# Kernel tuning notes

Measured on AMD Instinct MI355X. Metric: run time of the kernel, lower is better.

The kernel has to match this reference:

```python
import jax, jax.numpy as jnp
import numpy as np

B, S, D, H = 4, 1024, 768, 12
DH = D // H  # 64
ALPHA = 0.5
EPS = 1e-12


def setup_inputs() -> dict:
    key = jax.random.key(0)
    ks = jax.random.split(key, 12)
    s = 0.02
    return {
        "hidden_states": jax.random.normal(ks[0], (B, S, D), jnp.float32),
        "attention_mask": jnp.zeros((B, 1, 1, S), jnp.float32),
        "previous_attention": jax.random.uniform(ks[1], (B, H, S, S), jnp.float32),
        "Wq": jax.random.normal(ks[2], (D, D), jnp.float32) * s,
        "bq": jnp.zeros((D,), jnp.float32),
        "Wk": jax.random.normal(ks[3], (D, D), jnp.float32) * s,
        "bk": jnp.zeros((D,), jnp.float32),
        "Wv": jax.random.normal(ks[4], (D, D), jnp.float32) * s,
        "bv": jnp.zeros((D,), jnp.float32),
        "conv_w": jax.random.normal(ks[5], (H, H), jnp.float32) * 0.1,  # 1x1 conv over head channels
        "conv_b": jnp.zeros((H,), jnp.float32),
        "Wo": jax.random.normal(ks[6], (D, D), jnp.float32) * s,
        "bo": jnp.zeros((D,), jnp.float32),
        "ln_w": jnp.ones((D,), jnp.float32),
        "ln_b": jnp.zeros((D,), jnp.float32),
    }


def _split_heads(x):
    # [B,S,D] -> [B,H,S,DH]
    return x.reshape(B, S, H, DH).transpose(0, 2, 1, 3)


def reference(hidden_states, attention_mask, previous_attention,
              Wq, bq, Wk, bk, Wv, bv, conv_w, conv_b, Wo, bo, ln_w, ln_b):
    q = _split_heads(hidden_states @ Wq + bq)
    k = _split_heads(hidden_states @ Wk + bk)
    v = _split_heads(hidden_states @ Wv + bv)

    scores = jnp.einsum('bhqd,bhkd->bhqk', q, k) / jnp.sqrt(jnp.float32(DH))
    scores = scores + attention_mask
    probs = jax.nn.softmax(scores, axis=-1)

    # 1x1 conv over head channels on previous attention, mix, re-softmax
    prev = jnp.einsum('oi,biqk->boqk', conv_w, previous_attention) + conv_b[None, :, None, None]
    probs = jax.nn.softmax(ALPHA * prev + (1.0 - ALPHA) * probs, axis=-1)

    ctx = jnp.einsum('bhqk,bhkd->bhqd', probs, v)
    ctx = ctx.transpose(0, 2, 1, 3).reshape(B, S, D)

    out = ctx @ Wo + bo
    out = out + hidden_states
    u = out.mean(-1, keepdims=True)
    var = ((out - u) ** 2).mean(-1, keepdims=True)
    out = (out - u) / jnp.sqrt(var + EPS)
    return ln_w * out + ln_b
```

## Files before the change

### kernel.cpp

```cpp
#include <hip/hip_runtime.h>
#include <math.h>

#define BB 4
#define SS 1024
#define DD 768
#define HH 12
#define DHH 64

typedef __attribute__((ext_vector_type(8))) short bf16x8;
typedef __attribute__((ext_vector_type(4))) float f32x4;

__device__ __forceinline__ unsigned int f2bf(float f) {
    unsigned int u = __float_as_uint(f);
    return (u + 0x7FFFu + ((u >> 16) & 1u)) >> 16;
}
__device__ __forceinline__ float bf2f(unsigned int h) {
    return __uint_as_float(h << 16);
}

__device__ __forceinline__ void glds16(const void* g, void* l) {
    __builtin_amdgcn_global_load_lds(
        (const __attribute__((address_space(1))) void*)g,
        (__attribute__((address_space(3))) void*)l, 16, 0, 0);
}

__global__ __launch_bounds__(256)
void cvt_hidden_kernel(const float* __restrict__ src, unsigned short* __restrict__ dst)
{
    const int idx = (blockIdx.x * 256 + threadIdx.x) * 8;
    float4 a = *(const float4*)&src[idx];
    float4 b = *(const float4*)&src[idx + 4];
    uint4 p;
    p.x = f2bf(a.x) | (f2bf(a.y) << 16);
    p.y = f2bf(a.z) | (f2bf(a.w) << 16);
    p.z = f2bf(b.x) | (f2bf(b.y) << 16);
    p.w = f2bf(b.z) | (f2bf(b.w) << 16);
    *(uint4*)&dst[idx] = p;
}

__global__ __launch_bounds__(256)
void transpose_w_kernel(const float* __restrict__ Wq, const float* __restrict__ Wk,
                        const float* __restrict__ Wv, const float* __restrict__ Wo,
                        unsigned short* __restrict__ Wt)
{
    __shared__ float tile[32][33];
    const int t = threadIdx.x;
    const int kt = blockIdx.x, nt = blockIdx.y, w = blockIdx.z;
    const float* src = (w == 0) ? Wq : (w == 1) ? Wk : (w == 2) ? Wv : Wo;
    const int r = t >> 3, c4 = (t & 7) * 4;
    float4 v = *(const float4*)&src[(kt * 32 + r) * DD + nt * 32 + c4];
    tile[r][c4 + 0] = v.x; tile[r][c4 + 1] = v.y;
    tile[r][c4 + 2] = v.z; tile[r][c4 + 3] = v.w;
    __syncthreads();
    uint2 p;
    p.x = f2bf(tile[c4 + 0][r]) | (f2bf(tile[c4 + 1][r]) << 16);
    p.y = f2bf(tile[c4 + 2][r]) | (f2bf(tile[c4 + 3][r]) << 16);
    *(uint2*)&Wt[((size_t)w * DD + nt * 32 + r) * DD + kt * 32 + c4] = p;
}

__device__ __forceinline__ void gemm_core64(
    const char* __restrict__ Ag, const char* __restrict__ Bg,
    char* As, char* Bs, int tid, f32x4 (&acc)[2][2])
{
    const int lane = tid & 63;
    const int wr = (tid >> 7) & 1;
    const int wc = (tid >> 6) & 1;
    const int ldst = (tid & 192) << 4;

    for (int c = 0; c < 12; ++c) {
        const int kbyte = c * 128;
        #pragma unroll
        for (int i = 0; i < 2; ++i) {
            const int s = i * 256 + tid;
            const int row = s >> 3, kb = s & 7;
            const size_t off = (size_t)row * 1536 + kbyte + ((kb ^ (row & 7)) << 4);
            glds16(Ag + off, As + i * 4096 + ldst);
            glds16(Bg + off, Bs + i * 4096 + ldst);
        }
        __syncthreads();
        #pragma unroll
        for (int ks = 0; ks < 2; ++ks) {
            const int kb = ks * 4 + (lane >> 4);
            bf16x8 a[2], b[2];
            #pragma unroll
            for (int mi = 0; mi < 2; ++mi) {
                const int row = wr * 32 + mi * 16 + (lane & 15);
                a[mi] = *(const bf16x8*)(As + row * 128 + ((kb ^ (row & 7)) << 4));
            }
            #pragma unroll
            for (int ni = 0; ni < 2; ++ni) {
                const int row = wc * 32 + ni * 16 + (lane & 15);
                b[ni] = *(const bf16x8*)(Bs + row * 128 + ((kb ^ (row & 7)) << 4));
            }
            #pragma unroll
            for (int mi = 0; mi < 2; ++mi)
                #pragma unroll
                for (int ni = 0; ni < 2; ++ni)
                    acc[mi][ni] = __builtin_amdgcn_mfma_f32_16x16x32_bf16(
                        a[mi], b[ni], acc[mi][ni], 0, 0, 0);
        }
        __syncthreads();
    }
}

__global__ __launch_bounds__(256)
void qkv_gemm_kernel(const unsigned short* __restrict__ hbf, const unsigned short* __restrict__ Wt,
                     const float* __restrict__ bq, const float* __restrict__ bk,
                     const float* __restrict__ bv,
                     unsigned short* __restrict__ Qb, unsigned short* __restrict__ Kb,
                     unsigned short* __restrict__ Vtb)
{
    __shared__ __align__(16) char As[8192];
    __shared__ __align__(16) char Bs[8192];
    const int tid = threadIdx.x;
    const int m0 = blockIdx.x * 64;
    const int w = blockIdx.y / 12;
    const int n0w = (blockIdx.y % 12) * 64;

    f32x4 acc[2][2];
    const f32x4 z4 = {0.f, 0.f, 0.f, 0.f};
    acc[0][0] = z4; acc[0][1] = z4; acc[1][0] = z4; acc[1][1] = z4;

    const char* Ag = (const char*)hbf + (size_t)m0 * 1536;
    const char* Bg = (const char*)Wt + ((size_t)w * DD + n0w) * 1536;
    gemm_core64(Ag, Bg, As, Bs, tid, acc);

    const int lane = tid & 63;
    const int wr = (tid >> 7) & 1, wc = (tid >> 6) & 1;
    const int b = m0 >> 10, s0 = m0 & 1023;
    const int h = n0w >> 6;
    const float* bias = (w == 0) ? bq : (w == 1) ? bk : bv;

    if (w == 2) {
        #pragma unroll
        for (int mi = 0; mi < 2; ++mi)
            #pragma unroll
            for (int ni = 0; ni < 2; ++ni) {
                const int drow = wc * 32 + ni * 16 + (lane & 15);
                const float bb = bias[n0w + drow];
                #pragma unroll
                for (int r = 0; r < 4; ++r) {
                    const int scol = wr * 32 + mi * 16 + (lane >> 4) * 4 + r;
                    const int byte = (drow * 128 + scol * 2) ^ ((drow & 7) << 4);
                    *(unsigned short*)(As + byte) = (unsigned short)f2bf(acc[mi][ni][r] + bb);
                }
            }
        __syncthreads();
        const int drow = tid >> 2, c32 = (tid & 3) * 32;
        const int sw = (drow & 7) << 4;
        uint4 lo = *(uint4*)(As + ((drow * 128 + c32) ^ sw));
        uint4 hi = *(uint4*)(As + ((drow * 128 + c32 + 16) ^ sw));
        char* dst = (char*)Vtb + ((((size_t)(b * HH + h) * DHH) + drow) * SS + s0) * 2 + c32;
        *(uint4*)dst = lo; *(uint4*)(dst + 16) = hi;
    } else {
        #pragma unroll
        for (int mi = 0; mi < 2; ++mi)
            #pragma unroll
            for (int ni = 0; ni < 2; ++ni) {
                const int ncol = wc * 32 + ni * 16 + (lane & 15);
                const float bb = bias[n0w + ncol];
                #pragma unroll
                for (int r = 0; r < 4; ++r) {
                    const int srow = wr * 32 + mi * 16 + (lane >> 4) * 4 + r;
                    const int byte = (srow * 128 + ncol * 2) ^ ((srow & 7) << 4);
                    *(unsigned short*)(As + byte) = (unsigned short)f2bf(acc[mi][ni][r] + bb);
                }
            }
        __syncthreads();
        const int srow = tid >> 2, c32 = (tid & 3) * 32;
        const int sw = (srow & 7) << 4;
        uint4 lo = *(uint4*)(As + ((srow * 128 + c32) ^ sw));
        uint4 hi = *(uint4*)(As + ((srow * 128 + c32 + 16) ^ sw));
        unsigned short* base = (w == 0) ? Qb : Kb;
        char* dst = (char*)base + (((size_t)(b * HH + h) * SS + s0 + srow) * DHH) * 2 + c32;
        *(uint4*)dst = lo; *(uint4*)(dst + 16) = hi;
    }
}

__global__ __launch_bounds__(256)
void qk_exp_kernel(const unsigned short* __restrict__ Qb, const unsigned short* __restrict__ Kb,
                   const float* __restrict__ mask,
                   unsigned short* __restrict__ E1, float* __restrict__ Z1)
{
    __shared__ __align__(16) char Ks[32768];
    __shared__ __align__(16) char Es[8192];
    const int tid = threadIdx.x;
    const int lane = tid & 63;
    const int wv = tid >> 6;
    const int bh = blockIdx.x >> 4;
    const int q0 = (blockIdx.x & 15) * 64;
    const int b = bh / HH;
    const int qw = q0 + wv * 16;
    const int ldst = (tid & 192) << 4;

    const char* Qrow = (const char*)Qb + ((size_t)bh * SS + qw + (lane & 15)) * 128;
    bf16x8 aq0 = *(const bf16x8*)(Qrow + (lane >> 4) * 16);
    bf16x8 aq1 = *(const bf16x8*)(Qrow + 64 + (lane >> 4) * 16);

    float zr[4] = {0.f, 0.f, 0.f, 0.f};
    const char* Kbase = (const char*)Kb + (size_t)bh * SS * 128;

    for (int c = 0; c < 4; ++c) {
        #pragma unroll
        for (int i = 0; i < 8; ++i) {
            const int s = i * 256 + tid;
            const int row = s >> 3, kb = s & 7;
            glds16(Kbase + (size_t)(c * 256 + row) * 128 + ((kb ^ (row & 7)) << 4),
                   Ks + i * 4096 + ldst);
        }
        __syncthreads();
        for (int kg = 0; kg < 4; ++kg) {
            #pragma unroll
            for (int nfi = 0; nfi < 4; ++nfi) {
                const int nf = kg * 4 + nfi;
                const int krow = nf * 16 + (lane & 15);
                const int kx = krow & 7;
                bf16x8 b0 = *(const bf16x8*)(Ks + krow * 128 + (((lane >> 4) ^ kx) << 4));
                bf16x8 b1 = *(const bf16x8*)(Ks + krow * 128 + (((4 + (lane >> 4)) ^ kx) << 4));
                f32x4 accf = {0.f, 0.f, 0.f, 0.f};
                accf = __builtin_amdgcn_mfma_f32_16x16x32_bf16(aq0, b0, accf, 0, 0, 0);
                accf = __builtin_amdgcn_mfma_f32_16x16x32_bf16(aq1, b1, accf, 0, 0, 0);
                const int kcol = c * 256 + krow;
                const float mk = mask[b * SS + kcol];
                const int kl = nfi * 16 + (lane & 15);
                #pragma unroll
                for (int r = 0; r < 4; ++r) {
                    const int ql = wv * 16 + (lane >> 4) * 4 + r;
                    const float e = __expf(accf[r] * 0.125f + mk);
                    zr[r] += e;
                    const int byte = (ql * 128 + kl * 2) ^ ((ql & 7) << 4);
                    *(unsigned short*)(Es + byte) = (unsigned short)f2bf(e);
                }
            }
            __syncthreads();
            {
                const int ql = tid >> 2, c32 = (tid & 3) * 32;
                const int sw = (ql & 7) << 4;
                uint4 lo = *(uint4*)(Es + ((ql * 128 + c32) ^ sw));
                uint4 hi = *(uint4*)(Es + ((ql * 128 + c32 + 16) ^ sw));
                char* dst = (char*)E1 + ((size_t)bh * SS + q0 + ql) * 2048
                          + (c * 256 + kg * 64) * 2 + c32;
                *(uint4*)dst = lo; *(uint4*)(dst + 16) = hi;
            }
            __syncthreads();
        }
    }

    #pragma unroll
    for (int r = 0; r < 4; ++r) {
        float z = zr[r];
        z += __shfl_xor(z, 1); z += __shfl_xor(z, 2);
        z += __shfl_xor(z, 4); z += __shfl_xor(z, 8);
        if ((lane & 15) == 0)
            Z1[(size_t)bh * SS + qw + (lane >> 4) * 4 + r] = z;
    }
}

__global__ __launch_bounds__(256)
void e2_kernel(unsigned short* __restrict__ E1, const float* __restrict__ Z1,
               const float* __restrict__ prev, const float* __restrict__ cw,
               const float* __restrict__ cb, float* __restrict__ Z2)
{
    __shared__ float cws[144], cbs[12], izs[12], zred[4][12];
    const int t = threadIdx.x;
    const int b = blockIdx.x >> 10;
    const int q = blockIdx.x & 1023;

    if (t < 144) cws[t] = cw[t];
    if (t < 12) {
        cbs[t] = cb[t];
        izs[t] = 1.0f / Z1[((size_t)(b * HH + t)) * SS + q];
    }
    __syncthreads();

    float z2[12];
    #pragma unroll
    for (int h = 0; h < 12; ++h) z2[h] = 0.f;

    #pragma unroll
    for (int c = 0; c < 2; ++c) {
        const int k = c * 512 + t * 2;
        float2 pv[12];
        #pragma unroll
        for (int i = 0; i < 12; ++i)
            pv[i] = *(const float2*)&prev[(((size_t)(b * HH + i)) * SS + q) * SS + k];
        const size_t e1base = (((size_t)(b * HH)) * SS + q) * SS + k;
        #pragma unroll
        for (int h = 0; h < 12; ++h) {
            float mix0 = cbs[h], mix1 = cbs[h];
            #pragma unroll
            for (int i = 0; i < 12; ++i) {
                mix0 = fmaf(cws[h * 12 + i], pv[i].x, mix0);
                mix1 = fmaf(cws[h * 12 + i], pv[i].y, mix1);
            }
            unsigned int u = *(unsigned int*)&E1[e1base + (size_t)h * SS * SS];
            const float p10 = bf2f(u & 0xFFFFu) * izs[h];
            const float p11 = bf2f(u >> 16) * izs[h];
            const float e0 = __expf(0.5f * (mix0 + p10));
            const float e1 = __expf(0.5f * (mix1 + p11));
            z2[h] += e0 + e1;
            *(unsigned int*)&E1[e1base + (size_t)h * SS * SS] = f2bf(e0) | (f2bf(e1) << 16);
        }
    }

    #pragma unroll
    for (int h = 0; h < 12; ++h) {
        float z = z2[h];
        for (int off = 32; off; off >>= 1) z += __shfl_xor(z, off);
        z2[h] = z;
    }
    if ((t & 63) == 0) {
        const int wv = t >> 6;
        #pragma unroll
        for (int h = 0; h < 12; ++h) zred[wv][h] = z2[h];
    }
    __syncthreads();
    if (t < 12)
        Z2[((size_t)(b * HH + t)) * SS + q] =
            zred[0][t] + zred[1][t] + zred[2][t] + zred[3][t];
}

__global__ __launch_bounds__(256)
void pv_kernel(const unsigned short* __restrict__ E2, const float* __restrict__ Z2,
               const unsigned short* __restrict__ Vtb, unsigned short* __restrict__ ctx)
{
    __shared__ __align__(16) char Es[8192];
    __shared__ __align__(16) char Vs[8192];
    const int tid = threadIdx.x;
    const int lane = tid & 63;
    const int wv = tid >> 6;
    const int bh = blockIdx.x >> 4;
    const int q0 = (blockIdx.x & 15) * 64;
    const int b = bh / HH, h = bh % HH;
    const int ldst = (tid & 192) << 4;

    f32x4 acc[4];
    const f32x4 z4 = {0.f, 0.f, 0.f, 0.f};
    acc[0] = z4; acc[1] = z4; acc[2] = z4; acc[3] = z4;

    const char* Ebase = (const char*)E2 + ((size_t)bh * SS + q0) * 2048;
    const char* Vbase = (const char*)Vtb + (size_t)bh * DHH * 2048;

    for (int c = 0; c < 16; ++c) {
        const int kbyte = c * 128;
        #pragma unroll
        for (int i = 0; i < 2; ++i) {
            const int s = i * 256 + tid;
            const int row = s >> 3, kb = s & 7;
            const size_t off = (size_t)row * 2048 + kbyte + ((kb ^ (row & 7)) << 4);
            glds16(Ebase + off, Es + i * 4096 + ldst);
            glds16(Vbase + off, Vs + i * 4096 + ldst);
        }
        __syncthreads();
        #pragma unroll
        for (int ks = 0; ks < 2; ++ks) {
            const int kb = ks * 4 + (lane >> 4);
            const int arow = wv * 16 + (lane & 15);
            bf16x8 a = *(const bf16x8*)(Es + arow * 128 + ((kb ^ (arow & 7)) << 4));
            #pragma unroll
            for (int nf = 0; nf < 4; ++nf) {
                const int vrow = nf * 16 + (lane & 15);
                bf16x8 bb = *(const bf16x8*)(Vs + vrow * 128 + ((kb ^ (vrow & 7)) << 4));
                acc[nf] = __builtin_amdgcn_mfma_f32_16x16x32_bf16(a, bb, acc[nf], 0, 0, 0);
            }
        }
        __syncthreads();
    }

    float iz[4];
    #pragma unroll
    for (int r = 0; r < 4; ++r)
        iz[r] = 1.0f / Z2[(size_t)bh * SS + q0 + wv * 16 + (lane >> 4) * 4 + r];

    #pragma unroll
    for (int nf = 0; nf < 4; ++nf) {
        const int d = nf * 16 + (lane & 15);
        #pragma unroll
        for (int r = 0; r < 4; ++r) {
            const int ql = wv * 16 + (lane >> 4) * 4 + r;
            const int byte = (ql * 128 + d * 2) ^ ((ql & 7) << 4);
            *(unsigned short*)(Es + byte) = (unsigned short)f2bf(acc[nf][r] * iz[r]);
        }
    }
    __syncthreads();
    {
        const int ql = tid >> 2, c32 = (tid & 3) * 32;
        const int sw = (ql & 7) << 4;
        uint4 lo = *(uint4*)(Es + ((ql * 128 + c32) ^ sw));
        uint4 hi = *(uint4*)(Es + ((ql * 128 + c32 + 16) ^ sw));
        char* dst = (char*)ctx + ((size_t)(b * SS + q0 + ql) * DD + h * DHH) * 2 + c32;
        *(uint4*)dst = lo; *(uint4*)(dst + 16) = hi;
    }
}

__global__ __launch_bounds__(256)
void o_gemm_kernel(const unsigned short* __restrict__ ctx, const unsigned short* __restrict__ WtO,
                   const float* __restrict__ bo, float* __restrict__ gout)
{
    __shared__ __align__(16) char smem[16384];
    char* As = smem;
    char* Bs = smem + 8192;
    const int tid = threadIdx.x;
    const int m0 = blockIdx.x * 64;
    const int n0 = blockIdx.y * 64;

    f32x4 acc[2][2];
    const f32x4 z4 = {0.f, 0.f, 0.f, 0.f};
    acc[0][0] = z4; acc[0][1] = z4; acc[1][0] = z4; acc[1][1] = z4;

    gemm_core64((const char*)ctx + (size_t)m0 * 1536,
                (const char*)WtO + (size_t)n0 * 1536, As, Bs, tid, acc);

    const int lane = tid & 63;
    const int wr = (tid >> 7) & 1, wc = (tid >> 6) & 1;
    #pragma unroll
    for (int mi = 0; mi < 2; ++mi)
        #pragma unroll
        for (int ni = 0; ni < 2; ++ni) {
            const int ncol = wc * 32 + ni * 16 + (lane & 15);
            const float bb = bo[n0 + ncol];
            #pragma unroll
            for (int r = 0; r < 4; ++r) {
                const int row = wr * 32 + mi * 16 + (lane >> 4) * 4 + r;
                *(float*)(smem + ((row * 256 + ncol * 4) ^ ((row & 7) << 4))) =
                    acc[mi][ni][r] + bb;
            }
        }
    __syncthreads();
    {
        const int row = tid >> 2, c64 = (tid & 3) * 64;
        const int sw = (row & 7) << 4;
        float4 v[4];
        #pragma unroll
        for (int j = 0; j < 4; ++j)
            v[j] = *(float4*)(smem + ((row * 256 + c64 + j * 16) ^ sw));
        float* dst = gout + (size_t)(m0 + row) * DD + n0 + (tid & 3) * 16;
        #pragma unroll
        for (int j = 0; j < 4; ++j)
            *(float4*)(dst + j * 4) = v[j];
    }
}

__global__ __launch_bounds__(256)
void ln_kernel(const float* __restrict__ go, const float* __restrict__ hid,
               const float* __restrict__ lw, const float* __restrict__ lb,
               float* __restrict__ out)
{
    const int row = blockIdx.x;
    const int tid = threadIdx.x;
    const int lane = tid & 63, wave = tid >> 6;
    __shared__ float wsum[4], wsq[4];

    float x[3];
    float ssum = 0.f, ssq = 0.f;
    #pragma unroll
    for (int j = 0; j < 3; ++j) {
        const int n = tid + j * 256;
        const float v = go[(size_t)row * DD + n] + hid[(size_t)row * DD + n];
        x[j] = v; ssum += v; ssq += v * v;
    }
    for (int off = 32; off; off >>= 1) {
        ssum += __shfl_xor(ssum, off);
        ssq  += __shfl_xor(ssq, off);
    }
    if (lane == 0) { wsum[wave] = ssum; wsq[wave] = ssq; }
    __syncthreads();
    const float tsum = wsum[0] + wsum[1] + wsum[2] + wsum[3];
    const float tsq  = wsq[0] + wsq[1] + wsq[2] + wsq[3];
    const float mean = tsum * (1.0f / 768.0f);
    const float var  = tsq * (1.0f / 768.0f) - mean * mean;
    const float rstd = rsqrtf(var + 1e-12f);
    #pragma unroll
    for (int j = 0; j < 3; ++j) {
        const int n = tid + j * 256;
        out[(size_t)row * DD + n] = lw[n] * ((x[j] - mean) * rstd) + lb[n];
    }
}

extern "C" void kernel_launch(void* const* d_in, const int* in_sizes, int n_in,
                              void* d_out, int out_size, void* d_ws, size_t ws_size,
                              hipStream_t stream)
{
    const float* hidden = (const float*)d_in[0];
    const float* mask   = (const float*)d_in[1];
    const float* prev   = (const float*)d_in[2];
    const float* Wq = (const float*)d_in[3];  const float* bq = (const float*)d_in[4];
    const float* Wk = (const float*)d_in[5];  const float* bk = (const float*)d_in[6];
    const float* Wv = (const float*)d_in[7];  const float* bv = (const float*)d_in[8];
    const float* cw = (const float*)d_in[9];  const float* cb = (const float*)d_in[10];
    const float* Wo = (const float*)d_in[11]; const float* bo = (const float*)d_in[12];
    const float* lw = (const float*)d_in[13]; const float* lb = (const float*)d_in[14];
    float* out = (float*)d_out;

    char* w = (char*)d_ws;
    unsigned short* hbf = (unsigned short*)(w);
    unsigned short* Wt  = (unsigned short*)(w + 6291456);
    unsigned short* Qb  = (unsigned short*)(w + 11010048);
    unsigned short* Kb  = (unsigned short*)(w + 17301504);
    unsigned short* Vtb = (unsigned short*)(w + 23592960);
    unsigned short* E1  = (unsigned short*)(w + 29884416);
    float* Z1 = (float*)(w + 130547712);
    float* Z2 = (float*)(w + 130744320);
    unsigned short* ctx = hbf;
    float* gout = (float*)(w + 11010048);

    dim3 blk(256);
    cvt_hidden_kernel<<<dim3(1536), blk, 0, stream>>>(hidden, hbf);
    transpose_w_kernel<<<dim3(24, 24, 4), blk, 0, stream>>>(Wq, Wk, Wv, Wo, Wt);
    qkv_gemm_kernel<<<dim3(64, 36), blk, 0, stream>>>(hbf, Wt, bq, bk, bv, Qb, Kb, Vtb);
    qk_exp_kernel<<<dim3(768), blk, 0, stream>>>(Qb, Kb, mask, E1, Z1);
    e2_kernel<<<dim3(4096), blk, 0, stream>>>(E1, Z1, prev, cw, cb, Z2);
    pv_kernel<<<dim3(768), blk, 0, stream>>>(E1, Z2, Vtb, ctx);
    o_gemm_kernel<<<dim3(64, 12), blk, 0, stream>>>(ctx, Wt + (size_t)3 * DD * DD, bo, gout);
    ln_kernel<<<dim3(4096), blk, 0, stream>>>(gout, hidden, lw, lb, out);
}
```

Measured before the change: 468.8 us.

## Fuse QK softmax, head-conv mixing, and PV into one attention kernel

Replaces the three-kernel pipeline (QK exp to E1, conv-mix re-exp in place, PV) with one kernel per (batch, 16-query tile). Each of 12 waves handles one head. A first pass recomputes QK scores to get the row sums, and a second pass rebuilds the probabilities in LDS, applies the 12x12 head mixing from previous_attention, and accumulates P·V. This removes the large bf16 E1 intermediate in global memory, which was written, read and rewritten. In exchange, QK^T is computed twice, and K and V are read straight from global memory without LDS staging. Only 256 blocks of 768 threads are launched, which may limit occupancy.

```diff
diff --git a/kernel.cpp b/kernel.cpp
--- a/kernel.cpp
+++ b/kernel.cpp
@@ -177,218 +177,167 @@
     }
 }
 
-__global__ __launch_bounds__(256)
-void qk_exp_kernel(const unsigned short* __restrict__ Qb, const unsigned short* __restrict__ Kb,
-                   const float* __restrict__ mask,
-                   unsigned short* __restrict__ E1, float* __restrict__ Z1)
-{
-    __shared__ __align__(16) char Ks[32768];
-    __shared__ __align__(16) char Es[8192];
-    const int tid = threadIdx.x;
+__global__ __launch_bounds__(768)
+void fused_attn_kernel(const unsigned short* __restrict__ Qb, const unsigned short* __restrict__ Kb,
+                       const unsigned short* __restrict__ Vtb, const float* __restrict__ prev,
+                       const float* __restrict__ mask, const float* __restrict__ cw,
+                       const float* __restrict__ cb, unsigned short* __restrict__ ctx)
+{
+    __shared__ __align__(16) char Pbuf[24576];
+    __shared__ float cws[144], cbs[12];
+    __shared__ float z2buf[12][16];
+
+    const int tid  = threadIdx.x;
     const int lane = tid & 63;
-    const int wv = tid >> 6;
-    const int bh = blockIdx.x >> 4;
-    const int q0 = (blockIdx.x & 15) * 64;
-    const int b = bh / HH;
-    const int qw = q0 + wv * 16;
-    const int ldst = (tid & 192) << 4;
-
-    const char* Qrow = (const char*)Qb + ((size_t)bh * SS + qw + (lane & 15)) * 128;
-    bf16x8 aq0 = *(const bf16x8*)(Qrow + (lane >> 4) * 16);
-    bf16x8 aq1 = *(const bf16x8*)(Qrow + 64 + (lane >> 4) * 16);
+    const int w    = tid >> 6;
+    const int b    = blockIdx.x >> 6;
+    const int q0   = (blockIdx.x & 63) * 16;
+
+    if (tid < 144) cws[tid] = cw[tid];
+    if (tid < 12)  cbs[tid] = cb[tid];
+
+    const int slot = tid & 255;
+    const int hgrp = tid >> 8;
+    const int qB   = slot >> 4;
+    const int k4   = slot & 15;
+
+    const char* Qrow = (const char*)Qb + (((size_t)(b * HH + w) * SS) + q0 + (lane & 15)) * 128;
+    const bf16x8 aq0 = *(const bf16x8*)(Qrow + (lane >> 4) * 16);
+    const bf16x8 aq1 = *(const bf16x8*)(Qrow + 64 + (lane >> 4) * 16);
+
+    const char* Kbase = (const char*)Kb + (size_t)(b * HH + w) * SS * 128;
+    const char* Vbase = (const char*)Vtb + (size_t)(b * HH + w) * DHH * 2048;
+
+    __syncthreads();
 
     float zr[4] = {0.f, 0.f, 0.f, 0.f};
-    const char* Kbase = (const char*)Kb + (size_t)bh * SS * 128;
-
-    for (int c = 0; c < 4; ++c) {
-        #pragma unroll
-        for (int i = 0; i < 8; ++i) {
-            const int s = i * 256 + tid;
-            const int row = s >> 3, kb = s & 7;
-            glds16(Kbase + (size_t)(c * 256 + row) * 128 + ((kb ^ (row & 7)) << 4),
-                   Ks + i * 4096 + ldst);
-        }
-        __syncthreads();
-        for (int kg = 0; kg < 4; ++kg) {
-            #pragma unroll
-            for (int nfi = 0; nfi < 4; ++nfi) {
-                const int nf = kg * 4 + nfi;
-                const int krow = nf * 16 + (lane & 15);
-                const int kx = krow & 7;
-                bf16x8 b0 = *(const bf16x8*)(Ks + krow * 128 + (((lane >> 4) ^ kx) << 4));
-                bf16x8 b1 = *(const bf16x8*)(Ks + krow * 128 + (((4 + (lane >> 4)) ^ kx) << 4));
-                f32x4 accf = {0.f, 0.f, 0.f, 0.f};
-                accf = __builtin_amdgcn_mfma_f32_16x16x32_bf16(aq0, b0, accf, 0, 0, 0);
-                accf = __builtin_amdgcn_mfma_f32_16x16x32_bf16(aq1, b1, accf, 0, 0, 0);
-                const int kcol = c * 256 + krow;
-                const float mk = mask[b * SS + kcol];
-                const int kl = nfi * 16 + (lane & 15);
-                #pragma unroll
-                for (int r = 0; r < 4; ++r) {
-                    const int ql = wv * 16 + (lane >> 4) * 4 + r;
-                    const float e = __expf(accf[r] * 0.125f + mk);
-                    zr[r] += e;
-                    const int byte = (ql * 128 + kl * 2) ^ ((ql & 7) << 4);
-                    *(unsigned short*)(Es + byte) = (unsigned short)f2bf(e);
-                }
-            }
-            __syncthreads();
-            {
-                const int ql = tid >> 2, c32 = (tid & 3) * 32;
-                const int sw = (ql & 7) << 4;
-                uint4 lo = *(uint4*)(Es + ((ql * 128 + c32) ^ sw));
-                uint4 hi = *(uint4*)(Es + ((ql * 128 + c32 + 16) ^ sw));
-                char* dst = (char*)E1 + ((size_t)bh * SS + q0 + ql) * 2048
-                          + (c * 256 + kg * 64) * 2 + c32;
-                *(uint4*)dst = lo; *(uint4*)(dst + 16) = hi;
-            }
-            __syncthreads();
-        }
-    }
-
+    for (int kt = 0; kt < 16; ++kt) {
+        #pragma unroll
+        for (int nf = 0; nf < 4; ++nf) {
+            const int krow = kt * 64 + nf * 16 + (lane & 15);
+            bf16x8 bk0 = *(const bf16x8*)(Kbase + (size_t)krow * 128 + (lane >> 4) * 16);
+            bf16x8 bk1 = *(const bf16x8*)(Kbase + (size_t)krow * 128 + 64 + (lane >> 4) * 16);
+            f32x4 s = {0.f, 0.f, 0.f, 0.f};
+            s = __builtin_amdgcn_mfma_f32_16x16x32_bf16(aq0, bk0, s, 0, 0, 0);
+            s = __builtin_amdgcn_mfma_f32_16x16x32_bf16(aq1, bk1, s, 0, 0, 0);
+            const float mk = mask[b * SS + krow];
+            #pragma unroll
+            for (int r = 0; r < 4; ++r)
+                zr[r] += __expf(s[r] * 0.125f + mk);
+        }
+    }
+    float invz1[4];
     #pragma unroll
     for (int r = 0; r < 4; ++r) {
         float z = zr[r];
         z += __shfl_xor(z, 1); z += __shfl_xor(z, 2);
         z += __shfl_xor(z, 4); z += __shfl_xor(z, 8);
-        if ((lane & 15) == 0)
-            Z1[(size_t)bh * SS + qw + (lane >> 4) * 4 + r] = z;
-    }
-}
-
-__global__ __launch_bounds__(256)
-void e2_kernel(unsigned short* __restrict__ E1, const float* __restrict__ Z1,
-               const float* __restrict__ prev, const float* __restrict__ cw,
-               const float* __restrict__ cb, float* __restrict__ Z2)
-{
-    __shared__ float cws[144], cbs[12], izs[12], zred[4][12];
-    const int t = threadIdx.x;
-    const int b = blockIdx.x >> 10;
-    const int q = blockIdx.x & 1023;
-
-    if (t < 144) cws[t] = cw[t];
-    if (t < 12) {
-        cbs[t] = cb[t];
-        izs[t] = 1.0f / Z1[((size_t)(b * HH + t)) * SS + q];
-    }
-    __syncthreads();
-
-    float z2[12];
-    #pragma unroll
-    for (int h = 0; h < 12; ++h) z2[h] = 0.f;
-
-    #pragma unroll
-    for (int c = 0; c < 2; ++c) {
-        const int k = c * 512 + t * 2;
-        float2 pv[12];
+        invz1[r] = 1.0f / z;
+    }
+
+    f32x4 pacc[4];
+    const f32x4 zz = {0.f, 0.f, 0.f, 0.f};
+    pacc[0] = zz; pacc[1] = zz; pacc[2] = zz; pacc[3] = zz;
+    float z2acc[4] = {0.f, 0.f, 0.f, 0.f};
+
+    for (int kt = 0; kt < 16; ++kt) {
+        #pragma unroll
+        for (int nf = 0; nf < 4; ++nf) {
+            const int krow = kt * 64 + nf * 16 + (lane & 15);
+            bf16x8 bk0 = *(const bf16x8*)(Kbase + (size_t)krow * 128 + (lane >> 4) * 16);
+            bf16x8 bk1 = *(const bf16x8*)(Kbase + (size_t)krow * 128 + 64 + (lane >> 4) * 16);
+            f32x4 s = {0.f, 0.f, 0.f, 0.f};
+            s = __builtin_amdgcn_mfma_f32_16x16x32_bf16(aq0, bk0, s, 0, 0, 0);
+            s = __builtin_amdgcn_mfma_f32_16x16x32_bf16(aq1, bk1, s, 0, 0, 0);
+            const float mk = mask[b * SS + krow];
+            const int kcl = nf * 16 + (lane & 15);
+            #pragma unroll
+            for (int r = 0; r < 4; ++r) {
+                const int qr = (lane >> 4) * 4 + r;
+                const float p1 = __expf(s[r] * 0.125f + mk) * invz1[r];
+                *(unsigned short*)(Pbuf + w * 2048 + ((qr * 128 + kcl * 2) ^ ((qr & 7) << 4))) =
+                    (unsigned short)f2bf(p1);
+            }
+        }
+        __syncthreads();
+
+        float4 pvv[12];
         #pragma unroll
         for (int i = 0; i < 12; ++i)
-            pv[i] = *(const float2*)&prev[(((size_t)(b * HH + i)) * SS + q) * SS + k];
-        const size_t e1base = (((size_t)(b * HH)) * SS + q) * SS + k;
-        #pragma unroll
-        for (int h = 0; h < 12; ++h) {
-            float mix0 = cbs[h], mix1 = cbs[h];
+            pvv[i] = *(const float4*)&prev[(((size_t)(b * HH + i)) * SS + q0 + qB) * SS + kt * 64 + k4 * 4];
+        #pragma unroll
+        for (int j = 0; j < 4; ++j) {
+            const int h = hgrp * 4 + j;
+            char* pp = Pbuf + ((h * 2048 + qB * 128 + k4 * 8) ^ ((qB & 7) << 4));
+            uint2 pu = *(uint2*)pp;
+            float m0 = cbs[h], m1 = cbs[h], m2 = cbs[h], m3 = cbs[h];
             #pragma unroll
             for (int i = 0; i < 12; ++i) {
-                mix0 = fmaf(cws[h * 12 + i], pv[i].x, mix0);
-                mix1 = fmaf(cws[h * 12 + i], pv[i].y, mix1);
-            }
-            unsigned int u = *(unsigned int*)&E1[e1base + (size_t)h * SS * SS];
-            const float p10 = bf2f(u & 0xFFFFu) * izs[h];
-            const float p11 = bf2f(u >> 16) * izs[h];
-            const float e0 = __expf(0.5f * (mix0 + p10));
-            const float e1 = __expf(0.5f * (mix1 + p11));
-            z2[h] += e0 + e1;
-            *(unsigned int*)&E1[e1base + (size_t)h * SS * SS] = f2bf(e0) | (f2bf(e1) << 16);
-        }
-    }
-
-    #pragma unroll
-    for (int h = 0; h < 12; ++h) {
-        float z = z2[h];
-        for (int off = 32; off; off >>= 1) z += __shfl_xor(z, off);
-        z2[h] = z;
-    }
-    if ((t & 63) == 0) {
-        const int wv = t >> 6;
-        #pragma unroll
-        for (int h = 0; h < 12; ++h) zred[wv][h] = z2[h];
-    }
-    __syncthreads();
-    if (t < 12)
-        Z2[((size_t)(b * HH + t)) * SS + q] =
-            zred[0][t] + zred[1][t] + zred[2][t] + zred[3][t];
-}
-
-__global__ __launch_bounds__(256)
-void pv_kernel(const unsigned short* __restrict__ E2, const float* __restrict__ Z2,
-               const unsigned short* __restrict__ Vtb, unsigned short* __restrict__ ctx)
-{
-    __shared__ __align__(16) char Es[8192];
-    __shared__ __align__(16) char Vs[8192];
-    const int tid = threadIdx.x;
-    const int lane = tid & 63;
-    const int wv = tid >> 6;
-    const int bh = blockIdx.x >> 4;
-    const int q0 = (blockIdx.x & 15) * 64;
-    const int b = bh / HH, h = bh % HH;
-    const int ldst = (tid & 192) << 4;
-
-    f32x4 acc[4];
-    const f32x4 z4 = {0.f, 0.f, 0.f, 0.f};
-    acc[0] = z4; acc[1] = z4; acc[2] = z4; acc[3] = z4;
-
-    const char* Ebase = (const char*)E2 + ((size_t)bh * SS + q0) * 2048;
-    const char* Vbase = (const char*)Vtb + (size_t)bh * DHH * 2048;
-
-    for (int c = 0; c < 16; ++c) {
-        const int kbyte = c * 128;
-        #pragma unroll
-        for (int i = 0; i < 2; ++i) {
-            const int s = i * 256 + tid;
-            const int row = s >> 3, kb = s & 7;
-            const size_t off = (size_t)row * 2048 + kbyte + ((kb ^ (row & 7)) << 4);
-            glds16(Ebase + off, Es + i * 4096 + ldst);
-            glds16(Vbase + off, Vs + i * 4096 + ldst);
-        }
-        __syncthreads();
+                const float cwi = cws[h * 12 + i];
+                m0 = fmaf(cwi, pvv[i].x, m0);
+                m1 = fmaf(cwi, pvv[i].y, m1);
+                m2 = fmaf(cwi, pvv[i].z, m2);
+                m3 = fmaf(cwi, pvv[i].w, m3);
+            }
+            const float e0 = __expf(0.5f * (m0 + bf2f(pu.x & 0xFFFFu)));
+            const float e1 = __expf(0.5f * (m1 + bf2f(pu.x >> 16)));
+            const float e2 = __expf(0.5f * (m2 + bf2f(pu.y & 0xFFFFu)));
+            const float e3 = __expf(0.5f * (m3 + bf2f(pu.y >> 16)));
+            z2acc[j] += (e0 + e1) + (e2 + e3);
+            uint2 ou;
+            ou.x = f2bf(e0) | (f2bf(e1) << 16);
+            ou.y = f2bf(e2) | (f2bf(e3) << 16);
+            *(uint2*)pp = ou;
+        }
+        __syncthreads();
+
         #pragma unroll
         for (int ks = 0; ks < 2; ++ks) {
-            const int kb = ks * 4 + (lane >> 4);
-            const int arow = wv * 16 + (lane & 15);
-            bf16x8 a = *(const bf16x8*)(Es + arow * 128 + ((kb ^ (arow & 7)) << 4));
-            #pragma unroll
-            for (int nf = 0; nf < 4; ++nf) {
-                const int vrow = nf * 16 + (lane & 15);
-                bf16x8 bb = *(const bf16x8*)(Vs + vrow * 128 + ((kb ^ (vrow & 7)) << 4));
-                acc[nf] = __builtin_amdgcn_mfma_f32_16x16x32_bf16(a, bb, acc[nf], 0, 0, 0);
-            }
-        }
-        __syncthreads();
-    }
-
-    float iz[4];
-    #pragma unroll
-    for (int r = 0; r < 4; ++r)
-        iz[r] = 1.0f / Z2[(size_t)bh * SS + q0 + wv * 16 + (lane >> 4) * 4 + r];
-
-    #pragma unroll
-    for (int nf = 0; nf < 4; ++nf) {
-        const int d = nf * 16 + (lane & 15);
+            const int q = lane & 15;
+            bf16x8 pa = *(const bf16x8*)(Pbuf + w * 2048 +
+                          ((q * 128 + ks * 64 + (lane >> 4) * 16) ^ ((q & 7) << 4)));
+            #pragma unroll
+            for (int nfd = 0; nfd < 4; ++nfd) {
+                const int vrow = nfd * 16 + (lane & 15);
+                bf16x8 vb = *(const bf16x8*)(Vbase + (size_t)vrow * 2048 + kt * 128 +
+                                             ks * 64 + (lane >> 4) * 16);
+                pacc[nfd] = __builtin_amdgcn_mfma_f32_16x16x32_bf16(pa, vb, pacc[nfd], 0, 0, 0);
+            }
+        }
+    }
+
+    #pragma unroll
+    for (int j = 0; j < 4; ++j) {
+        float z = z2acc[j];
+        z += __shfl_xor(z, 1); z += __shfl_xor(z, 2);
+        z += __shfl_xor(z, 4); z += __shfl_xor(z, 8);
+        z2acc[j] = z;
+    }
+    if ((tid & 15) == 0) {
+        #pragma unroll
+        for (int j = 0; j < 4; ++j)
+            z2buf[hgrp * 4 + j][qB] = z2acc[j];
+    }
+    __syncthreads();
+
+    #pragma unroll
+    for (int nfd = 0; nfd < 4; ++nfd) {
+        const int d = nfd * 16 + (lane & 15);
         #pragma unroll
         for (int r = 0; r < 4; ++r) {
-            const int ql = wv * 16 + (lane >> 4) * 4 + r;
-            const int byte = (ql * 128 + d * 2) ^ ((ql & 7) << 4);
-            *(unsigned short*)(Es + byte) = (unsigned short)f2bf(acc[nf][r] * iz[r]);
+            const int qr = (lane >> 4) * 4 + r;
+            const float o = pacc[nfd][r] / z2buf[w][qr];
+            *(unsigned short*)(Pbuf + w * 2048 + ((qr * 128 + d * 2) ^ ((qr & 7) << 4))) =
+                (unsigned short)f2bf(o);
         }
     }
     __syncthreads();
     {
-        const int ql = tid >> 2, c32 = (tid & 3) * 32;
-        const int sw = (ql & 7) << 4;
-        uint4 lo = *(uint4*)(Es + ((ql * 128 + c32) ^ sw));
-        uint4 hi = *(uint4*)(Es + ((ql * 128 + c32 + 16) ^ sw));
-        char* dst = (char*)ctx + ((size_t)(b * SS + q0 + ql) * DD + h * DHH) * 2 + c32;
+        const int qq = lane >> 2, c32 = (lane & 3) * 32;
+        const int sw = (qq & 7) << 4;
+        uint4 lo = *(uint4*)(Pbuf + w * 2048 + ((qq * 128 + c32) ^ sw));
+        uint4 hi = *(uint4*)(Pbuf + w * 2048 + ((qq * 128 + c32 + 16) ^ sw));
+        char* dst = (char*)ctx + (((size_t)(b * SS + q0 + qq)) * DD + w * DHH) * 2 + c32;
         *(uint4*)dst = lo; *(uint4*)(dst + 16) = hi;
     }
 }
@@ -498,9 +447,6 @@
     unsigned short* Qb  = (unsigned short*)(w + 11010048);
     unsigned short* Kb  = (unsigned short*)(w + 17301504);
     unsigned short* Vtb = (unsigned short*)(w + 23592960);
-    unsigned short* E1  = (unsigned short*)(w + 29884416);
-    float* Z1 = (float*)(w + 130547712);
-    float* Z2 = (float*)(w + 130744320);
     unsigned short* ctx = hbf;
     float* gout = (float*)(w + 11010048);
 
@@ -508,9 +454,7 @@
     cvt_hidden_kernel<<<dim3(1536), blk, 0, stream>>>(hidden, hbf);
     transpose_w_kernel<<<dim3(24, 24, 4), blk, 0, stream>>>(Wq, Wk, Wv, Wo, Wt);
     qkv_gemm_kernel<<<dim3(64, 36), blk, 0, stream>>>(hbf, Wt, bq, bk, bv, Qb, Kb, Vtb);
-    qk_exp_kernel<<<dim3(768), blk, 0, stream>>>(Qb, Kb, mask, E1, Z1);
-    e2_kernel<<<dim3(4096), blk, 0, stream>>>(E1, Z1, prev, cw, cb, Z2);
-    pv_kernel<<<dim3(768), blk, 0, stream>>>(E1, Z2, Vtb, ctx);
+    fused_attn_kernel<<<dim3(256), dim3(768), 0, stream>>>(Qb, Kb, Vtb, prev, mask, cw, cb, ctx);
     o_gemm_kernel<<<dim3(64, 12), blk, 0, stream>>>(ctx, Wt + (size_t)3 * DD * DD, bo, gout);
     ln_kernel<<<dim3(4096), blk, 0, stream>>>(gout, hidden, lw, lb, out);
 }
```

Measured after the change: 510.6 us. 1.09x slower.
